# Kernel optimization log

Hardware: AMD Instinct MI355X
Metric: run time of the kernel (lower is better)

## Reference

```python
import jax, jax.numpy as jnp
import numpy as np

N_NODES = 50000
N_EDGES = 600000
IN_CH = 128
HID_CH = 128
OUT_CH = 64
NUM_GRAPHS = 512


def _gcn_conv(x, W, b, src, dst, n):
    # PyG GCNConv (eval): h = D^{-1/2} (A + I) D^{-1/2} (x W) + b
    h = x @ W  # [N, C]
    loop = jnp.arange(n)
    s = jnp.concatenate([src, loop])  # add self-loops
    d = jnp.concatenate([dst, loop])
    deg = jax.ops.segment_sum(jnp.ones_like(d, dtype=h.dtype), d, num_segments=n)
    dinv = jnp.where(deg > 0, jax.lax.rsqrt(deg), 0.0)
    coef = dinv[s] * dinv[d]  # [E+N]
    msg = h[s] * coef[:, None]  # gather + scale
    out = jax.ops.segment_sum(msg, d, num_segments=n)  # scatter-add
    return out + b


def setup_inputs() -> dict:
    key = jax.random.key(0)
    ks = jax.random.split(key, 10)
    x = jax.random.normal(ks[0], (N_NODES, IN_CH), dtype=jnp.float32)
    edge_index = jax.random.randint(ks[1], (2, N_EDGES), 0, N_NODES, dtype=jnp.int64)
    batch = jnp.sort(jax.random.randint(ks[2], (N_NODES,), 0, NUM_GRAPHS, dtype=jnp.int64))
    sc1 = 1.0 / np.sqrt(IN_CH)
    sc2 = 1.0 / np.sqrt(HID_CH)
    W1 = jax.random.uniform(ks[3], (IN_CH, HID_CH), jnp.float32, -sc1, sc1)
    b1 = jnp.zeros((HID_CH,), jnp.float32)
    W2 = jax.random.uniform(ks[4], (HID_CH, HID_CH), jnp.float32, -sc2, sc2)
    b2 = jnp.zeros((HID_CH,), jnp.float32)
    Wlin = jax.random.uniform(ks[5], (HID_CH, OUT_CH), jnp.float32, -sc2, sc2)
    blin = jax.random.uniform(ks[6], (OUT_CH,), jnp.float32, -sc2, sc2)
    return {"x": x, "W1": W1, "b1": b1, "W2": W2, "b2": b2,
            "Wlin": Wlin, "blin": blin, "edge_index": edge_index, "batch": batch}


def reference(x, W1, b1, W2, b2, Wlin, blin, edge_index, batch):
    n = x.shape[0]
    src, dst = edge_index[0], edge_index[1]
    h = jax.nn.relu(_gcn_conv(x, W1, b1, src, dst, n))
    # dropout: identity in eval mode (training=False)
    h = jax.nn.relu(_gcn_conv(h, W2, b2, src, dst, n))
    # global mean pool over graphs
    summed = jax.ops.segment_sum(h, batch, num_segments=NUM_GRAPHS)
    cnt = jax.ops.segment_sum(jnp.ones((n,), h.dtype), batch, num_segments=NUM_GRAPHS)
    pooled = summed / jnp.maximum(cnt, 1.0)[:, None]
    return pooled @ Wlin + blin  # [NUM_GRAPHS, OUT_CH]
```

## Files before the change

kernel.cpp:

```cpp
#include <hip/hip_runtime.h>

#define N_NODES 50000
#define N_EDGES 600000
#define CH 128
#define NUM_GRAPHS 512
#define OUT_CH 64
#define DSH 6
#define DSTRIDE 64
#define PF_GROUPS 8
#define PF_SLICE (N_NODES / PF_GROUPS)
#define PF_CHUNKS ((N_EDGES + 255) / 256)

typedef unsigned int uint32;
typedef __attribute__((ext_vector_type(8))) short short8;
typedef __attribute__((ext_vector_type(4))) float floatx4;

__device__ __forceinline__ uint32 bfpack(float a, float b) {
    uint32 ua = __builtin_bit_cast(uint32, a);
    uint32 ub = __builtin_bit_cast(uint32, b);
    ua = (ua + 0x7fffu + ((ua >> 16) & 1u)) >> 16;
    ub = (ub + 0x7fffu + ((ub >> 16) & 1u)) >> 16;
    return (ub << 16) | ua;
}
__device__ __forceinline__ unsigned short bfr(float f) {
    uint32 u = __builtin_bit_cast(uint32, f);
    u = (u + 0x7fffu + ((u >> 16) & 1u)) >> 16;
    return (unsigned short)u;
}
__device__ __forceinline__ float bf_lo(uint32 v) {
    return __builtin_bit_cast(float, v << 16);
}
__device__ __forceinline__ float bf_hi(uint32 v) {
    return __builtin_bit_cast(float, v & 0xffff0000u);
}

__global__ void k_prep(const float* __restrict__ W1, const float* __restrict__ W2,
                       unsigned short* __restrict__ W1t, unsigned short* __restrict__ W2t,
                       int* __restrict__ cur) {
    int idx = blockIdx.x * 256 + threadIdx.x;
    if (idx < N_NODES) cur[idx] = 0;
    if (idx < 32768) {
        int mat = idx >> 14;
        int rem = idx & 16383;
        int k = rem >> 7, c = rem & 127;
        const float* W = mat ? W2 : W1;
        unsigned short* Wt = mat ? W2t : W1t;
        Wt[c * 128 + k] = bfr(W[k * 128 + c]);
    }
}

__global__ __launch_bounds__(256) void k_fill_part(const int* __restrict__ src,
                                                   const int* __restrict__ dst,
                                                   int* __restrict__ cur,
                                                   int* __restrict__ srcs) {
    int g = blockIdx.x & (PF_GROUPS - 1);
    int chunk = blockIdx.x >> 3;
    int e = chunk * 256 + threadIdx.x;
    if (e < N_EDGES) {
        int d = dst[e];
        if ((unsigned)(d - g * PF_SLICE) < (unsigned)PF_SLICE) {
            int s = src[e];
            int p = atomicAdd(&cur[d], 1);
            srcs[(d << DSH) + p] = s;
        }
    }
}

template <bool AF32>
__global__ __launch_bounds__(256, 2) void k_gemm(const void* __restrict__ Av,
                                                 const unsigned short* __restrict__ Wt,
                                                 const int* __restrict__ cur,
                                                 unsigned short* __restrict__ outb) {
    __shared__ __align__(16) unsigned short as_[128][136];
    __shared__ __align__(16) unsigned short bs[128][136];
    int tid = threadIdx.x;
    int row0 = blockIdx.x * 128;

    #pragma unroll
    for (int it = 0; it < 8; ++it) {
        int idx = it * 256 + tid;
        int r = idx >> 4, seg = idx & 15;
        int gr = min(row0 + r, N_NODES - 1);
        if (AF32) {
            const float4* ap = (const float4*)((const float*)Av + (size_t)gr * 128 + seg * 8);
            float4 v0 = ap[0], v1 = ap[1];
            uint4 pk;
            pk.x = bfpack(v0.x, v0.y); pk.y = bfpack(v0.z, v0.w);
            pk.z = bfpack(v1.x, v1.y); pk.w = bfpack(v1.z, v1.w);
            *(uint4*)&as_[r][seg * 8] = pk;
        } else {
            *(uint4*)&as_[r][seg * 8] =
                *(const uint4*)((const unsigned short*)Av + (size_t)gr * 128 + seg * 8);
        }
    }
    #pragma unroll
    for (int it = 0; it < 8; ++it) {
        int idx = it * 256 + tid;
        int c = idx >> 4, seg = idx & 15;
        *(uint4*)&bs[c][seg * 8] = *(const uint4*)&Wt[c * 128 + seg * 8];
    }
    __syncthreads();

    int w = tid >> 6, lane = tid & 63, q = lane >> 4, m = lane & 15;
    int q8 = q * 8;
    floatx4 acc[2][8];
    #pragma unroll
    for (int rt = 0; rt < 2; ++rt)
        #pragma unroll
        for (int ct = 0; ct < 8; ++ct) {
            floatx4 z = {0.f, 0.f, 0.f, 0.f};
            acc[rt][ct] = z;
        }

    #pragma unroll
    for (int kc = 0; kc < 128; kc += 32) {
        short8 a0 = *(const short8*)&as_[w * 32 + m][kc + q8];
        short8 a1 = *(const short8*)&as_[w * 32 + 16 + m][kc + q8];
        #pragma unroll
        for (int ct = 0; ct < 8; ++ct) {
            short8 b = *(const short8*)&bs[ct * 16 + m][kc + q8];
            acc[0][ct] = __builtin_amdgcn_mfma_f32_16x16x32_bf16(a0, b, acc[0][ct], 0, 0, 0);
            acc[1][ct] = __builtin_amdgcn_mfma_f32_16x16x32_bf16(a1, b, acc[1][ct], 0, 0, 0);
        }
    }

    #pragma unroll
    for (int rt = 0; rt < 2; ++rt) {
        #pragma unroll
        for (int i = 0; i < 4; ++i) {
            int gr = row0 + w * 32 + rt * 16 + q * 4 + i;
            if (gr < N_NODES) {
                float sc = rsqrtf((float)(cur[gr] + 1));
                #pragma unroll
                for (int ct = 0; ct < 8; ++ct) {
                    outb[(size_t)gr * 128 + ct * 16 + m] = bfr(acc[rt][ct][i] * sc);
                }
            }
        }
    }
}

template <bool BF16OUT>
__global__ __launch_bounds__(256) void k_agg(const uint32* __restrict__ hb,
                                             const int* __restrict__ cnt_arr,
                                             const int* __restrict__ srcs,
                                             const float* __restrict__ bias,
                                             void* __restrict__ outv) {
    int node = __builtin_amdgcn_readfirstlane(blockIdx.x * 4 + (threadIdx.x >> 6));
    int lane = threadIdx.x & 63;

    int cnt = cnt_arr[node];
    float dn = rsqrtf((float)(cnt + 1));
    uint32 vs = hb[node * 64 + lane];
    float ax = bf_lo(vs), ay = bf_hi(vs);

    int start = node << DSH;
    int last = start + cnt - 1;
    for (int j = 0; j < cnt; j += 8) {
        int i0 = start + j;
        int i1 = min(i0 + 1, last);
        int i2 = min(i0 + 2, last);
        int i3 = min(i0 + 3, last);
        int i4 = min(i0 + 4, last);
        int i5 = min(i0 + 5, last);
        int i6 = min(i0 + 6, last);
        int i7 = min(i0 + 7, last);
        int s0 = srcs[i0], s1 = srcs[i1], s2 = srcs[i2], s3 = srcs[i3];
        int s4 = srcs[i4], s5 = srcs[i5], s6 = srcs[i6], s7 = srcs[i7];
        uint32 v0 = hb[s0 * 64 + lane];
        uint32 v1 = hb[s1 * 64 + lane];
        uint32 v2 = hb[s2 * 64 + lane];
        uint32 v3 = hb[s3 * 64 + lane];
        uint32 v4 = hb[s4 * 64 + lane];
        uint32 v5 = hb[s5 * 64 + lane];
        uint32 v6 = hb[s6 * 64 + lane];
        uint32 v7 = hb[s7 * 64 + lane];
        int rem = cnt - j;
        v1 = (rem > 1) ? v1 : 0u;
        v2 = (rem > 2) ? v2 : 0u;
        v3 = (rem > 3) ? v3 : 0u;
        v4 = (rem > 4) ? v4 : 0u;
        v5 = (rem > 5) ? v5 : 0u;
        v6 = (rem > 6) ? v6 : 0u;
        v7 = (rem > 7) ? v7 : 0u;
        ax += bf_lo(v0); ay += bf_hi(v0);
        ax += bf_lo(v1); ay += bf_hi(v1);
        ax += bf_lo(v2); ay += bf_hi(v2);
        ax += bf_lo(v3); ay += bf_hi(v3);
        ax += bf_lo(v4); ay += bf_hi(v4);
        ax += bf_lo(v5); ay += bf_hi(v5);
        ax += bf_lo(v6); ay += bf_hi(v6);
        ax += bf_lo(v7); ay += bf_hi(v7);
    }
    float2 b = ((const float2*)bias)[lane];
    ax = fmaxf(ax * dn + b.x, 0.f);
    ay = fmaxf(ay * dn + b.y, 0.f);
    if (BF16OUT) ((uint32*)outv)[node * 64 + lane] = bfpack(ax, ay);
    else         ((float2*)outv)[node * 64 + lane] = make_float2(ax, ay);
}

__global__ __launch_bounds__(256) void k_pool_linear(const float* __restrict__ h,
                                                     const int* __restrict__ batch,
                                                     const float* __restrict__ Wl,
                                                     const float* __restrict__ bl,
                                                     float* __restrict__ out) {
    __shared__ int sb[2];
    __shared__ float4 sacc[256];
    __shared__ float xr[CH];
    __shared__ float po[4][OUT_CH];
    int g = blockIdx.x;
    int tid = threadIdx.x;
    if (tid < 2) {
        int target = g + tid;
        int lo = 0, hi = N_NODES;
        while (lo < hi) {
            int mid = (lo + hi) >> 1;
            if (batch[mid] < target) lo = mid + 1; else hi = mid;
        }
        sb[tid] = lo;
    }
    __syncthreads();
    int lo = sb[0], hi = sb[1];
    int q = tid & 31;
    int r = tid >> 5;
    const float4* h4 = (const float4*)h;
    float4 acc = make_float4(0.f, 0.f, 0.f, 0.f);
    for (int i = lo + r; i < hi; i += 8) {
        float4 v = h4[(size_t)i * 32 + q];
        acc.x += v.x; acc.y += v.y; acc.z += v.z; acc.w += v.w;
    }
    sacc[tid] = acc;
    __syncthreads();
    if (r == 0) {
        #pragma unroll
        for (int p = 1; p < 8; ++p) {
            float4 t = sacc[q + p * 32];
            acc.x += t.x; acc.y += t.y; acc.z += t.z; acc.w += t.w;
        }
        float inv = 1.f / (float)((hi - lo) > 0 ? (hi - lo) : 1);
        xr[q * 4 + 0] = acc.x * inv;
        xr[q * 4 + 1] = acc.y * inv;
        xr[q * 4 + 2] = acc.z * inv;
        xr[q * 4 + 3] = acc.w * inv;
    }
    __syncthreads();
    int c = tid & 63;
    int kh = tid >> 6;
    float o = 0.f;
    #pragma unroll 8
    for (int k = kh * 32; k < kh * 32 + 32; ++k) o += xr[k] * Wl[k * OUT_CH + c];
    po[kh][c] = o;
    __syncthreads();
    if (tid < OUT_CH) {
        float v = bl[tid] + po[0][tid] + po[1][tid] + po[2][tid] + po[3][tid];
        out[g * OUT_CH + tid] = v;
    }
}

extern "C" void kernel_launch(void* const* d_in, const int* in_sizes, int n_in,
                              void* d_out, int out_size, void* d_ws, size_t ws_size,
                              hipStream_t stream) {
    const float* x    = (const float*)d_in[0];
    const float* W1   = (const float*)d_in[1];
    const float* b1   = (const float*)d_in[2];
    const float* W2   = (const float*)d_in[3];
    const float* b2   = (const float*)d_in[4];
    const float* Wlin = (const float*)d_in[5];
    const float* blin = (const float*)d_in[6];
    const int* ei     = (const int*)d_in[7];
    const int* batch  = (const int*)d_in[8];
    const int* esrc = ei;
    const int* edst = ei + N_EDGES;
    float* out = (float*)d_out;

    char* w = (char*)d_ws;
    size_t o = 0;
    float* hA            = (float*)(w + o);          o += (size_t)N_NODES * CH * 4;
    unsigned short* hb   = (unsigned short*)(w + o); o += (size_t)N_NODES * CH * 2;
    uint32* habf         = (uint32*)(w + o);         o += (size_t)N_NODES * 64 * 4;
    unsigned short* W1t  = (unsigned short*)(w + o); o += 16384 * 2;
    unsigned short* W2t  = (unsigned short*)(w + o); o += 16384 * 2;
    int* srcs            = (int*)(w + o);            o += (size_t)N_NODES * DSTRIDE * 4;
    int* cur             = (int*)(w + o);            o += 200704;
    (void)ws_size; (void)in_sizes; (void)n_in; (void)out_size;

    dim3 b256(256);
    k_prep<<<dim3(196), b256, 0, stream>>>(W1, W2, W1t, W2t, cur);
    k_fill_part<<<dim3(PF_GROUPS * PF_CHUNKS), b256, 0, stream>>>(esrc, edst, cur, srcs);

    dim3 gG((N_NODES + 127) / 128);
    dim3 gA(N_NODES / 4);
    k_gemm<true><<<gG, b256, 0, stream>>>(x, W1t, cur, hb);
    k_agg<true><<<gA, b256, 0, stream>>>((const uint32*)hb, cur, srcs, b1, habf);
    k_gemm<false><<<gG, b256, 0, stream>>>(habf, W2t, cur, hb);
    k_agg<false><<<gA, b256, 0, stream>>>((const uint32*)hb, cur, srcs, b2, hA);
    k_pool_linear<<<dim3(NUM_GRAPHS), b256, 0, stream>>>(hA, batch, Wlin, blin, out);
}
```

Baseline: 195.2 us.

## Split aggregation into channel quarters with 8 edges per wavefront

The aggregation kernel now gives each wavefront one node and a quarter of its channels (grid y = 4). Lanes form 8 groups, each reading 8 bytes per lane for a different neighbor edge, and the partial sums are then reduced with cross-lane shuffles. This replaces the serial 8-edge unrolled loop over the full 128-channel row. The aim is more parallel memory requests in flight per wave and fewer loop iterations, at the cost of 4x more blocks, repeated index and count loads, shuffle reductions, and only one lane group doing the final store.

Result: slower. 278.9 us (+42.9%).

```diff
diff --git a/kernel.cpp b/kernel.cpp
--- a/kernel.cpp
+++ b/kernel.cpp
@@ -141,62 +141,60 @@
 }
 
 template <bool BF16OUT>
-__global__ __launch_bounds__(256) void k_agg(const uint32* __restrict__ hb,
-                                             const int* __restrict__ cnt_arr,
-                                             const int* __restrict__ srcs,
-                                             const float* __restrict__ bias,
-                                             void* __restrict__ outv) {
+__global__ __launch_bounds__(256) void k_agg_q(const uint32* __restrict__ hb,
+                                               const int* __restrict__ cnt_arr,
+                                               const int* __restrict__ srcs,
+                                               const float* __restrict__ bias,
+                                               void* __restrict__ outv) {
     int node = __builtin_amdgcn_readfirstlane(blockIdx.x * 4 + (threadIdx.x >> 6));
+    int q    = __builtin_amdgcn_readfirstlane(blockIdx.y);
     int lane = threadIdx.x & 63;
+    int grp = lane >> 3;
+    int c   = lane & 7;
 
     int cnt = cnt_arr[node];
     float dn = rsqrtf((float)(cnt + 1));
-    uint32 vs = hb[node * 64 + lane];
-    float ax = bf_lo(vs), ay = bf_hi(vs);
-
+    const uint2* hb2 = (const uint2*)hb;
+    int qoff = q * 8 + c;
+
+    uint2 vs = hb2[(size_t)node * 32 + qoff];
+
+    float ax0 = 0.f, ay0 = 0.f, ax1 = 0.f, ay1 = 0.f;
     int start = node << DSH;
-    int last = start + cnt - 1;
+    int cl = cnt - 1;
     for (int j = 0; j < cnt; j += 8) {
-        int i0 = start + j;
-        int i1 = min(i0 + 1, last);
-        int i2 = min(i0 + 2, last);
-        int i3 = min(i0 + 3, last);
-        int i4 = min(i0 + 4, last);
-        int i5 = min(i0 + 5, last);
-        int i6 = min(i0 + 6, last);
-        int i7 = min(i0 + 7, last);
-        int s0 = srcs[i0], s1 = srcs[i1], s2 = srcs[i2], s3 = srcs[i3];
-        int s4 = srcs[i4], s5 = srcs[i5], s6 = srcs[i6], s7 = srcs[i7];
-        uint32 v0 = hb[s0 * 64 + lane];
-        uint32 v1 = hb[s1 * 64 + lane];
-        uint32 v2 = hb[s2 * 64 + lane];
-        uint32 v3 = hb[s3 * 64 + lane];
-        uint32 v4 = hb[s4 * 64 + lane];
-        uint32 v5 = hb[s5 * 64 + lane];
-        uint32 v6 = hb[s6 * 64 + lane];
-        uint32 v7 = hb[s7 * 64 + lane];
-        int rem = cnt - j;
-        v1 = (rem > 1) ? v1 : 0u;
-        v2 = (rem > 2) ? v2 : 0u;
-        v3 = (rem > 3) ? v3 : 0u;
-        v4 = (rem > 4) ? v4 : 0u;
-        v5 = (rem > 5) ? v5 : 0u;
-        v6 = (rem > 6) ? v6 : 0u;
-        v7 = (rem > 7) ? v7 : 0u;
-        ax += bf_lo(v0); ay += bf_hi(v0);
-        ax += bf_lo(v1); ay += bf_hi(v1);
-        ax += bf_lo(v2); ay += bf_hi(v2);
-        ax += bf_lo(v3); ay += bf_hi(v3);
-        ax += bf_lo(v4); ay += bf_hi(v4);
-        ax += bf_lo(v5); ay += bf_hi(v5);
-        ax += bf_lo(v6); ay += bf_hi(v6);
-        ax += bf_lo(v7); ay += bf_hi(v7);
-    }
-    float2 b = ((const float2*)bias)[lane];
-    ax = fmaxf(ax * dn + b.x, 0.f);
-    ay = fmaxf(ay * dn + b.y, 0.f);
-    if (BF16OUT) ((uint32*)outv)[node * 64 + lane] = bfpack(ax, ay);
-    else         ((float2*)outv)[node * 64 + lane] = make_float2(ax, ay);
+        int p = j + grp;
+        int s = srcs[start + min(p, cl)];
+        uint2 v = hb2[(size_t)s * 32 + qoff];
+        if (p >= cnt) { v.x = 0u; v.y = 0u; }
+        ax0 += bf_lo(v.x); ay0 += bf_hi(v.x);
+        ax1 += bf_lo(v.y); ay1 += bf_hi(v.y);
+    }
+
+    ax0 += __shfl_xor(ax0, 8, 64); ax0 += __shfl_xor(ax0, 16, 64); ax0 += __shfl_xor(ax0, 32, 64);
+    ay0 += __shfl_xor(ay0, 8, 64); ay0 += __shfl_xor(ay0, 16, 64); ay0 += __shfl_xor(ay0, 32, 64);
+    ax1 += __shfl_xor(ax1, 8, 64); ax1 += __shfl_xor(ax1, 16, 64); ax1 += __shfl_xor(ax1, 32, 64);
+    ay1 += __shfl_xor(ay1, 8, 64); ay1 += __shfl_xor(ay1, 16, 64); ay1 += __shfl_xor(ay1, 32, 64);
+
+    ax0 += bf_lo(vs.x); ay0 += bf_hi(vs.x);
+    ax1 += bf_lo(vs.y); ay1 += bf_hi(vs.y);
+
+    float4 b = *(const float4*)&bias[q * 32 + c * 4];
+    float r0 = fmaxf(ax0 * dn + b.x, 0.f);
+    float r1 = fmaxf(ay0 * dn + b.y, 0.f);
+    float r2 = fmaxf(ax1 * dn + b.z, 0.f);
+    float r3 = fmaxf(ay1 * dn + b.w, 0.f);
+
+    if (grp == 0) {
+        if (BF16OUT) {
+            uint2 pk;
+            pk.x = bfpack(r0, r1);
+            pk.y = bfpack(r2, r3);
+            ((uint2*)outv)[(size_t)node * 32 + qoff] = pk;
+        } else {
+            ((float4*)outv)[(size_t)node * 32 + qoff] = make_float4(r0, r1, r2, r3);
+        }
+    }
 }
 
 __global__ __launch_bounds__(256) void k_pool_linear(const float* __restrict__ h,
@@ -289,10 +287,10 @@
     k_fill_part<<<dim3(PF_GROUPS * PF_CHUNKS), b256, 0, stream>>>(esrc, edst, cur, srcs);
 
     dim3 gG((N_NODES + 127) / 128);
-    dim3 gA(N_NODES / 4);
+    dim3 gAq(N_NODES / 4, 4);
     k_gemm<true><<<gG, b256, 0, stream>>>(x, W1t, cur, hb);
-    k_agg<true><<<gA, b256, 0, stream>>>((const uint32*)hb, cur, srcs, b1, habf);
+    k_agg_q<true><<<gAq, b256, 0, stream>>>((const uint32*)hb, cur, srcs, b1, habf);
     k_gemm<false><<<gG, b256, 0, stream>>>(habf, W2t, cur, hb);
-    k_agg<false><<<gA, b256, 0, stream>>>((const uint32*)hb, cur, srcs, b2, hA);
+    k_agg_q<false><<<gAq, b256, 0, stream>>>((const uint32*)hb, cur, srcs, b2, hA);
     k_pool_linear<<<dim3(NUM_GRAPHS), b256, 0, stream>>>(hA, batch, Wlin, blin, out);
 }
```

## Replace partitioned atomic CSR fill with two-pass bucket binning

Applied to the files above, without the earlier changes.

Replaces the single edge-fill pass with two passes. The old pass launched 8 groups of blocks, each rescanning every edge and doing a global atomic per destination. The first new pass bins edges into 98 buckets of 512 destination nodes, using shared-memory histograms and one global atomic per bucket per block. The second pass gives each bucket to one block, which builds the per-node adjacency lists with shared-memory atomics and writes the counts. This removes the eightfold rereading of the edge list and most contended global atomics, at the cost of an extra intermediate buffer and fixed bucket capacities (8192 edges per bucket) that could drop edges on skewed inputs.

Measured after the change: 191.0 us. 1.02x faster.

```diff
diff --git a/kernel.cpp b/kernel.cpp
--- a/kernel.cpp
+++ b/kernel.cpp
@@ -7,9 +7,11 @@
 #define OUT_CH 64
 #define DSH 6
 #define DSTRIDE 64
-#define PF_GROUPS 8
-#define PF_SLICE (N_NODES / PF_GROUPS)
-#define PF_CHUNKS ((N_EDGES + 255) / 256)
+#define BSHIFT 9
+#define NBUCK 98
+#define BCAP 8192
+#define L1_EPT 16
+#define L1_BLOCKS ((N_EDGES + 256 * L1_EPT - 1) / (256 * L1_EPT))
 
 typedef unsigned int uint32;
 typedef __attribute__((ext_vector_type(8))) short short8;
@@ -36,9 +38,9 @@
 
 __global__ void k_prep(const float* __restrict__ W1, const float* __restrict__ W2,
                        unsigned short* __restrict__ W1t, unsigned short* __restrict__ W2t,
-                       int* __restrict__ cur) {
+                       int* __restrict__ gcnt) {
     int idx = blockIdx.x * 256 + threadIdx.x;
-    if (idx < N_NODES) cur[idx] = 0;
+    if (idx < NBUCK) gcnt[idx] = 0;
     if (idx < 32768) {
         int mat = idx >> 14;
         int rem = idx & 16383;
@@ -49,20 +51,67 @@
     }
 }
 
-__global__ __launch_bounds__(256) void k_fill_part(const int* __restrict__ src,
-                                                   const int* __restrict__ dst,
-                                                   int* __restrict__ cur,
-                                                   int* __restrict__ srcs) {
-    int g = blockIdx.x & (PF_GROUPS - 1);
-    int chunk = blockIdx.x >> 3;
-    int e = chunk * 256 + threadIdx.x;
-    if (e < N_EDGES) {
-        int d = dst[e];
-        if ((unsigned)(d - g * PF_SLICE) < (unsigned)PF_SLICE) {
-            int s = src[e];
-            int p = atomicAdd(&cur[d], 1);
-            srcs[(d << DSH) + p] = s;
-        }
+__global__ __launch_bounds__(256) void k_bin(const int* __restrict__ src,
+                                             const int* __restrict__ dst,
+                                             int* __restrict__ gcnt,
+                                             uint2* __restrict__ binned) {
+    __shared__ int hist[NBUCK];
+    __shared__ int base[NBUCK];
+    __shared__ int curs[NBUCK];
+    int tid = threadIdx.x;
+    if (tid < NBUCK) { hist[tid] = 0; curs[tid] = 0; }
+    __syncthreads();
+
+    int e0 = blockIdx.x * (256 * L1_EPT) + tid;
+    int ss[L1_EPT], dd[L1_EPT];
+    #pragma unroll
+    for (int i = 0; i < L1_EPT; ++i) {
+        int e = e0 + i * 256;
+        if (e < N_EDGES) {
+            ss[i] = src[e];
+            dd[i] = dst[e];
+            atomicAdd(&hist[dd[i] >> BSHIFT], 1);
+        } else {
+            dd[i] = -1;
+        }
+    }
+    __syncthreads();
+    if (tid < NBUCK) base[tid] = atomicAdd(&gcnt[tid], hist[tid]);
+    __syncthreads();
+    #pragma unroll
+    for (int i = 0; i < L1_EPT; ++i) {
+        if (dd[i] >= 0) {
+            int b = dd[i] >> BSHIFT;
+            int slot = base[b] + atomicAdd(&curs[b], 1);
+            if (slot < BCAP)
+                binned[(size_t)b * BCAP + slot] = make_uint2((uint32)ss[i], (uint32)dd[i]);
+        }
+    }
+}
+
+__global__ __launch_bounds__(256) void k_build(const uint2* __restrict__ binned,
+                                               const int* __restrict__ gcnt,
+                                               int* __restrict__ cur,
+                                               int* __restrict__ srcs) {
+    __shared__ int cl[1 << BSHIFT];
+    int b = blockIdx.x;
+    int tid = threadIdx.x;
+    #pragma unroll
+    for (int i = tid; i < (1 << BSHIFT); i += 256) cl[i] = 0;
+    __syncthreads();
+    int n = min(gcnt[b], BCAP);
+    int nb = b << BSHIFT;
+    for (int i = tid; i < n; i += 256) {
+        uint2 e = binned[(size_t)b * BCAP + i];
+        int d = (int)e.y;
+        int p = atomicAdd(&cl[d - nb], 1);
+        if (p < DSTRIDE) srcs[(d << DSH) + p] = (int)e.x;
+    }
+    __syncthreads();
+    #pragma unroll
+    for (int i = tid; i < (1 << BSHIFT); i += 256) {
+        int d = nb + i;
+        if (d < N_NODES) cur[d] = cl[i];
     }
 }
 
@@ -282,11 +331,14 @@
     unsigned short* W2t  = (unsigned short*)(w + o); o += 16384 * 2;
     int* srcs            = (int*)(w + o);            o += (size_t)N_NODES * DSTRIDE * 4;
     int* cur             = (int*)(w + o);            o += 200704;
+    uint2* binned        = (uint2*)(w + o);          o += (size_t)NBUCK * BCAP * 8;
+    int* gcnt            = (int*)(w + o);            o += 512;
     (void)ws_size; (void)in_sizes; (void)n_in; (void)out_size;
 
     dim3 b256(256);
-    k_prep<<<dim3(196), b256, 0, stream>>>(W1, W2, W1t, W2t, cur);
-    k_fill_part<<<dim3(PF_GROUPS * PF_CHUNKS), b256, 0, stream>>>(esrc, edst, cur, srcs);
+    k_prep<<<dim3(196), b256, 0, stream>>>(W1, W2, W1t, W2t, gcnt);
+    k_bin<<<dim3(L1_BLOCKS), b256, 0, stream>>>(esrc, edst, gcnt, binned);
+    k_build<<<dim3(NBUCK), b256, 0, stream>>>(binned, gcnt, cur, srcs);
 
     dim3 gG((N_NODES + 127) / 128);
     dim3 gA(N_NODES / 4);
```
